# Kernel optimization log

Measured on AMD Instinct MI355X. Metric: run time of the kernel, lower is better.

The kernel has to match this reference:

```python
import jax, jax.numpy as jnp
import numpy as np

H = 128          # hidden_size == in_channels == graph_hidden_size
P = 16           # pair_neurons
B = 4096         # number of graph pairs
T = 262144       # total nodes per side
V_D, V_P, V_A = 10000, 4000, 4000          # leaf vocab sizes
NG_D, NG_P, NG_A = 13000, 5200, 5200       # DAG graph node counts
L_D, L_P, L_A = 4, 4, 5                    # ancestor levels
TOTAL_V = V_D + V_P + V_A                  # 18000 rows in all_embedding


def setup_inputs() -> dict:
    key = jax.random.key(0)
    ks = jax.random.split(key, 40)
    n = lambda i, shape, s: jax.random.normal(ks[i], shape, jnp.float32) * s
    ri = lambda i, shape, hi: jax.random.randint(ks[i], shape, 0, hi, dtype=jnp.int64)
    inp = {}
    # forward args
    inp["left_x"] = ri(0, (T, 1), TOTAL_V)
    inp["left_graph_index"] = ri(1, (B,), B)
    inp["right_x"] = ri(2, (T, 1), TOTAL_V)
    inp["right_graph_index"] = ri(3, (B,), B)
    inp["left_x_batch"] = jnp.sort(ri(4, (T,), B))
    inp["right_x_batch"] = jnp.sort(ri(5, (T,), B))
    inp["left_diag_cnt"] = ri(6, (B,), 64)
    inp["right_diag_cnt"] = ri(7, (B,), 64)
    # DAG structure buffers (built by build_ancestors in the original)
    inp["anc_d"] = ri(8, (V_D, L_D), NG_D)
    inp["leaf_d"] = ri(9, (V_D, L_D), NG_D)
    inp["anc_p"] = ri(10, (V_P, L_P), NG_P)
    inp["leaf_p"] = ri(11, (V_P, L_P), NG_P)
    inp["anc_a"] = ri(12, (V_A, L_A), NG_A)
    inp["leaf_a"] = ri(13, (V_A, L_A), NG_A)
    # learned parameters
    inp["emb_d"] = n(14, (NG_D, H), 0.1)
    inp["emb_p"] = n(15, (NG_P, H), 0.1)
    inp["emb_a"] = n(16, (NG_A, H), 0.1)
    inp["Wl_d"] = n(17, (H, 2 * H), 0.05); inp["bl_d"] = n(18, (H,), 0.05); inp["ap_d"] = n(19, (H, 1), 0.05)
    inp["Wl_p"] = n(20, (H, 2 * H), 0.05); inp["bl_p"] = n(21, (H,), 0.05); inp["ap_p"] = n(22, (H, 1), 0.05)
    inp["Wl_a"] = n(23, (H, 2 * H), 0.05); inp["bl_a"] = n(24, (H,), 0.05); inp["ap_a"] = n(25, (H, 1), 0.05)
    inp["W_ntn"] = n(26, (H, H, P), 0.02)
    inp["V_ntn"] = n(27, (P, 2 * H), 0.02)
    inp["b_ntn"] = n(28, (P,), 0.02)
    inp["w_fc"] = n(29, (1, P), 0.1)
    inp["b_fc"] = n(30, (1,), 0.1)
    return inp


def _dag_embedding(emb, anc, leaf, Wl, bl, ap):
    # emb: [Ng,H]; anc/leaf: [V,L] int
    anc_e = emb[anc]    # [V,L,H]
    leaf_e = emb[leaf]  # [V,L,H]
    h = jnp.tanh(jnp.concatenate([anc_e, leaf_e], axis=-1) @ Wl.T + bl)  # [V,L,H]
    aw = (h @ ap)[..., 0]                     # [V,L]
    s = jax.nn.softmax(aw, axis=-1)           # [V,L]
    # torch.matmul((V,L),(V,L,C)).sum(dim=1) == einsum('l,vlc->vc', s.sum(0), anc_e)
    return jnp.einsum('l,vlc->vc', s.sum(axis=0), anc_e)  # [V,H]


def reference(left_x, left_graph_index, right_x, right_graph_index,
              left_x_batch, right_x_batch, left_diag_cnt, right_diag_cnt,
              anc_d, leaf_d, anc_p, leaf_p, anc_a, leaf_a,
              emb_d, emb_p, emb_a,
              Wl_d, bl_d, ap_d, Wl_p, bl_p, ap_p, Wl_a, bl_a, ap_a,
              W_ntn, V_ntn, b_ntn, w_fc, b_fc):
    all_emb = jnp.concatenate([
        _dag_embedding(emb_d, anc_d, leaf_d, Wl_d, bl_d, ap_d),
        _dag_embedding(emb_p, anc_p, leaf_p, Wl_p, bl_p, ap_p),
        _dag_embedding(emb_a, anc_a, leaf_a, Wl_a, bl_a, ap_a),
    ], axis=0)                                  # [TOTAL_V, H]
    left_onto = all_emb[left_x[:, 0]]           # [T,H]
    right_onto = all_emb[right_x[:, 0]]         # [T,H]
    le = jax.ops.segment_sum(left_onto, left_x_batch, num_segments=B)    # [B,H]
    re = jax.ops.segment_sum(right_onto, right_x_batch, num_segments=B)  # [B,H]
    # Neural tensor similarity: tanh(e1^T W_k e2 + V [e1;e2] + b)
    bilinear = jnp.einsum('bi,ijp,bj->bp', le, W_ntn, re)                # [B,P]
    block = jnp.concatenate([le, re], axis=-1) @ V_ntn.T                 # [B,P]
    pair_sim = jnp.tanh(bilinear + block + b_ntn)                        # [B,P]
    out = jax.nn.sigmoid(pair_sim @ w_fc.T + b_fc)[:, 0]                 # [B]
    return out
```

## Files before the change

### kernel.cpp

```cpp
#include <hip/hip_runtime.h>
#include <hip/hip_bf16.h>

typedef __hip_bfloat16 bf16;
typedef __attribute__((ext_vector_type(8))) short bf16x8;
typedef __attribute__((ext_vector_type(4))) float f32x4;

#define HID 128
#define PD  16
#define BB  4096
#define TT  262144
#define VD  10000
#define VP  4000
#define VA  4000
#define NGD 13000
#define NGP 5200
#define NGA 5200

#define NB_D ((NGD + 31) / 32)
#define NB_P ((NGP + 31) / 32)
#define NB_A ((NGA + 31) / 32)

__device__ __forceinline__ float2 bf2x(unsigned int u) {
    float lo = __uint_as_float(u << 16);
    float hi = __uint_as_float(u & 0xffff0000u);
    return make_float2(lo, hi);
}

union Pack2 { bf16 h[2]; unsigned int u; };
__device__ __forceinline__ unsigned int pk2(float a, float b) {
    Pack2 p; p.h[0] = __float2bfloat16(a); p.h[1] = __float2bfloat16(b); return p.u;
}

__global__ __launch_bounds__(256) void prep_b3(
    const float* __restrict__ Wl_d, const float* __restrict__ Wl_p, const float* __restrict__ Wl_a,
    bf16* __restrict__ B3_d, bf16* __restrict__ B3_p, bf16* __restrict__ B3_a)
{
    const int sec = blockIdx.x >> 4, jt = blockIdx.x & 15;
    const float* Wl = (sec == 0) ? Wl_d : (sec == 1) ? Wl_p : Wl_a;
    bf16* B3 = (sec == 0) ? B3_d : (sec == 1) ? B3_p : B3_a;
    const int tid = threadIdx.x;
    const int q = tid >> 6, lane = tid & 63;
    const int quad = lane >> 4, m = lane & 15;
    const int col = jt * 16 + m;
    const float* src = (col < 128) ? (Wl + col * 256) : (Wl + (col - 128) * 256 + 128);
    unsigned int pk[4];
#pragma unroll
    for (int jp = 0; jp < 4; ++jp) {
        int k0 = q * 32 + quad * 8 + 2 * jp;
        pk[jp] = pk2(src[k0], src[k0 + 1]);
    }
    uint4 val = make_uint4(pk[0], pk[1], pk[2], pk[3]);
    *reinterpret_cast<uint4*>(B3 + ((size_t)(jt * 4 + q) * 64 + lane) * 8) = val;
}

__device__ __forceinline__ void stage1_body(
    unsigned short (*Abf)[136],
    const float* __restrict__ emb, const bf16* __restrict__ B3,
    bf16* __restrict__ U, int NG, int blk)
{
    const int tid  = threadIdx.x;
    const int row0 = blk * 32;
    {
        const int r = tid >> 3, seg = tid & 7;
        const int g = row0 + r;
        float v[16];
        if (g < NG) {
            const float4* src = reinterpret_cast<const float4*>(emb + (size_t)g * HID + seg * 16);
#pragma unroll
            for (int i = 0; i < 4; ++i) {
                float4 f = src[i];
                v[4 * i] = f.x; v[4 * i + 1] = f.y; v[4 * i + 2] = f.z; v[4 * i + 3] = f.w;
            }
        } else {
#pragma unroll
            for (int i = 0; i < 16; ++i) v[i] = 0.f;
        }
        unsigned int pk[8];
#pragma unroll
        for (int i = 0; i < 8; ++i) pk[i] = pk2(v[2 * i], v[2 * i + 1]);
        uint4* dst = reinterpret_cast<uint4*>(&Abf[r][seg * 16]);
        dst[0] = make_uint4(pk[0], pk[1], pk[2], pk[3]);
        dst[1] = make_uint4(pk[4], pk[5], pk[6], pk[7]);
    }
    __syncthreads();

    const int lane   = tid & 63;
    const int w      = tid >> 6;
    const int gtile  = w & 1;
    const int jstrip = w >> 1;
    const int lrow   = gtile * 16 + (lane & 15);
    const int koff   = (lane >> 4) * 8;
    const bf16x8* B3f = reinterpret_cast<const bf16x8*>(B3);

    f32x4 acc[8];
#pragma unroll
    for (int t = 0; t < 8; ++t) acc[t] = (f32x4){0.f, 0.f, 0.f, 0.f};

#pragma unroll
    for (int q = 0; q < 4; ++q) {
        bf16x8 ef = *reinterpret_cast<const bf16x8*>(&Abf[lrow][q * 32 + koff]);
#pragma unroll
        for (int t = 0; t < 8; ++t) {
            int jt = jstrip * 8 + t;
            bf16x8 wf = B3f[(jt * 4 + q) * 64 + lane];
            acc[t] = __builtin_amdgcn_mfma_f32_16x16x32_bf16(wf, ef, acc[t], 0, 0, 0);
        }
    }

    const int g = row0 + gtile * 16 + (lane & 15);
    if (g < NG) {
        const int quad = lane >> 4;
        bf16* Ur = U + (size_t)g * 256;
#pragma unroll
        for (int t = 0; t < 8; ++t) {
            int j0 = (jstrip * 8 + t) * 16 + quad * 4;
            uint2 st = make_uint2(pk2(acc[t].x, acc[t].y), pk2(acc[t].z, acc[t].w));
            *reinterpret_cast<uint2*>(Ur + j0) = st;
        }
    }
}

__global__ __launch_bounds__(256) void stage1_mfma(
    const float* __restrict__ emb_d, const bf16* __restrict__ B3_d, bf16* __restrict__ U_d,
    const float* __restrict__ emb_p, const bf16* __restrict__ B3_p, bf16* __restrict__ U_p,
    const float* __restrict__ emb_a, const bf16* __restrict__ B3_a, bf16* __restrict__ U_a)
{
    __shared__ unsigned short Abf[32][136];
    int bx = blockIdx.x;
    if (bx < NB_D)             stage1_body(Abf, emb_d, B3_d, U_d, NGD, bx);
    else if (bx < NB_D + NB_P) stage1_body(Abf, emb_p, B3_p, U_p, NGP, bx - NB_D);
    else                       stage1_body(Abf, emb_a, B3_a, U_a, NGA, bx - NB_D - NB_P);
}

template <int L>
__device__ __forceinline__ void aw_body(
    float* sacc,
    const bf16* __restrict__ U, const int* __restrict__ anc, const int* __restrict__ leaf,
    const float* __restrict__ bl, const float* __restrict__ ap,
    float* __restrict__ s_out, int V, int blk, int nblk)
{
    const int tid  = threadIdx.x;
    const int lane = tid & 63;
    const int wid  = blk * 4 + (tid >> 6);
    const int nw   = nblk * 4;
    const float2 blv = *reinterpret_cast<const float2*>(bl + 2 * lane);
    const float2 apv = *reinterpret_cast<const float2*>(ap + 2 * lane);
    const unsigned int* Uw = reinterpret_cast<const unsigned int*>(U);
    float wacc[L];
#pragma unroll
    for (int l = 0; l < L; ++l) wacc[l] = 0.f;

    for (int v = wid; v < V; v += nw) {
        float aw[L];
#pragma unroll
        for (int l = 0; l < L; ++l) {
            int a = anc[v * L + l];
            int f = leaf[v * L + l];
            float2 a2 = bf2x(Uw[(size_t)a * 128 + lane]);
            float2 l2 = bf2x(Uw[(size_t)f * 128 + 64 + lane]);
            float t0 = tanhf(a2.x + l2.x + blv.x);
            float t1 = tanhf(a2.y + l2.y + blv.y);
            float p = t0 * apv.x + t1 * apv.y;
#pragma unroll
            for (int off = 32; off; off >>= 1) p += __shfl_xor(p, off, 64);
            aw[l] = p;
        }
        float m = aw[0];
#pragma unroll
        for (int l = 1; l < L; ++l) m = fmaxf(m, aw[l]);
        float den = 0.f, e[L];
#pragma unroll
        for (int l = 0; l < L; ++l) { e[l] = __expf(aw[l] - m); den += e[l]; }
        float inv = 1.f / den;
#pragma unroll
        for (int l = 0; l < L; ++l) wacc[l] += e[l] * inv;
    }
    if (lane == 0) {
#pragma unroll
        for (int l = 0; l < L; ++l) atomicAdd(&sacc[l], wacc[l]);
    }
    __syncthreads();
    if (tid < L) atomicAdd(&s_out[tid], sacc[tid]);
}

__global__ __launch_bounds__(256) void aw_all(
    const bf16* __restrict__ U_d, const int* __restrict__ anc_d, const int* __restrict__ leaf_d,
    const float* __restrict__ bl_d, const float* __restrict__ ap_d,
    const bf16* __restrict__ U_p, const int* __restrict__ anc_p, const int* __restrict__ leaf_p,
    const float* __restrict__ bl_p, const float* __restrict__ ap_p,
    const bf16* __restrict__ U_a, const int* __restrict__ anc_a, const int* __restrict__ leaf_a,
    const float* __restrict__ bl_a, const float* __restrict__ ap_a,
    float* __restrict__ s_sum)
{
    __shared__ float sacc[5];
    const int tid = threadIdx.x;
    if (tid < 5) sacc[tid] = 0.f;
    __syncthreads();
    int bx = blockIdx.x;
    if (bx < 512)      aw_body<4>(sacc, U_d, anc_d, leaf_d, bl_d, ap_d, s_sum + 0, VD, bx, 512);
    else if (bx < 768) aw_body<4>(sacc, U_p, anc_p, leaf_p, bl_p, ap_p, s_sum + 4, VP, bx - 512, 256);
    else               aw_body<5>(sacc, U_a, anc_a, leaf_a, bl_a, ap_a, s_sum + 8, VA, bx - 768, 256);
}

template <int L>
__device__ __forceinline__ void allemb_body(
    const float* __restrict__ emb, const int* __restrict__ anc,
    const float* __restrict__ s, float* __restrict__ out, int V, int blk, int nblk)
{
    const int tid   = threadIdx.x;
    const int lane4 = tid & 31;
    const int vslot = tid >> 5;
    const float4* emb4 = reinterpret_cast<const float4*>(emb);
    float4* out4 = reinterpret_cast<float4*>(out);
    float sv[L];
#pragma unroll
    for (int l = 0; l < L; ++l) sv[l] = s[l];
    for (int v = blk * 8 + vslot; v < V; v += nblk * 8) {
        float4 a = make_float4(0.f, 0.f, 0.f, 0.f);
#pragma unroll
        for (int l = 0; l < L; ++l) {
            float4 e = emb4[(size_t)anc[v * L + l] * 32 + lane4];
            a.x += sv[l] * e.x; a.y += sv[l] * e.y;
            a.z += sv[l] * e.z; a.w += sv[l] * e.w;
        }
        out4[(size_t)v * 32 + lane4] = a;
    }
}

__global__ __launch_bounds__(256) void allemb_all(
    const float* __restrict__ emb_d, const int* __restrict__ anc_d,
    const float* __restrict__ emb_p, const int* __restrict__ anc_p,
    const float* __restrict__ emb_a, const int* __restrict__ anc_a,
    const float* __restrict__ s_sum, float* __restrict__ all_emb)
{
    int bx = blockIdx.x;
    if (bx < 512)
        allemb_body<4>(emb_d, anc_d, s_sum + 0, all_emb, VD, bx, 512);
    else if (bx < 768)
        allemb_body<4>(emb_p, anc_p, s_sum + 4, all_emb + (size_t)VD * HID, VP, bx - 512, 256);
    else
        allemb_body<5>(emb_a, anc_a, s_sum + 8, all_emb + (size_t)(VD + VP) * HID, VA, bx - 768, 256);
}

__global__ __launch_bounds__(256) void seg_bounds(
    const int* __restrict__ lb, const int* __restrict__ rb,
    int* __restrict__ segL, int* __restrict__ segR)
{
    int gid = blockIdx.x * 256 + threadIdx.x;
    const int* batch;
    int* segp;
    int b;
    if (gid <= BB) { batch = lb; segp = segL; b = gid; }
    else if (gid <= 2 * BB + 1) { batch = rb; segp = segR; b = gid - BB - 1; }
    else return;
    int l = 0, r = TT;
    while (l < r) { int m = (l + r) >> 1; if (batch[m] < b) l = m + 1; else r = m; }
    segp[b] = l;
}

__global__ __launch_bounds__(256) void segsum_f4(
    const float* __restrict__ all_emb,
    const int* __restrict__ lx, const int* __restrict__ segL, float* __restrict__ le,
    const int* __restrict__ rx, const int* __restrict__ segR, float* __restrict__ re)
{
    __shared__ float4 red[8][32];
    const int tid = threadIdx.x;
    const int b   = blockIdx.x & (BB - 1);
    const int* x;
    const int* seg;
    float* out;
    if (blockIdx.x < BB) { x = lx; seg = segL; out = le; }
    else                 { x = rx; seg = segR; out = re; }
    const int lo = seg[b], hi = seg[b + 1];
    const int lane4 = tid & 31;
    const int slot  = tid >> 5;
    const float4* AE4 = reinterpret_cast<const float4*>(all_emb);
    float4 acc = make_float4(0.f, 0.f, 0.f, 0.f);
    int t = lo + slot;
    for (; t + 8 < hi; t += 16) {
        int i0 = x[t], i1 = x[t + 8];
        float4 v0 = AE4[(size_t)i0 * 32 + lane4];
        float4 v1 = AE4[(size_t)i1 * 32 + lane4];
        acc.x += v0.x; acc.y += v0.y; acc.z += v0.z; acc.w += v0.w;
        acc.x += v1.x; acc.y += v1.y; acc.z += v1.z; acc.w += v1.w;
    }
    for (; t < hi; t += 8) {
        float4 v0 = AE4[(size_t)x[t] * 32 + lane4];
        acc.x += v0.x; acc.y += v0.y; acc.z += v0.z; acc.w += v0.w;
    }
    red[slot][lane4] = acc;
    __syncthreads();
    if (slot < 4) {
        float4 o = red[slot + 4][lane4];
        acc.x += o.x; acc.y += o.y; acc.z += o.z; acc.w += o.w;
        red[slot][lane4] = acc;
    }
    __syncthreads();
    if (slot < 2) {
        float4 o = red[slot + 2][lane4];
        acc.x += o.x; acc.y += o.y; acc.z += o.z; acc.w += o.w;
        red[slot][lane4] = acc;
    }
    __syncthreads();
    if (slot == 0) {
        float4 o = red[1][lane4];
        acc.x += o.x; acc.y += o.y; acc.z += o.z; acc.w += o.w;
        reinterpret_cast<float4*>(out)[(size_t)b * 32 + lane4] = acc;
    }
}

__global__ __launch_bounds__(256) void ntn_part(
    const float* __restrict__ le, const float* __restrict__ re,
    const float* __restrict__ W2, float* __restrict__ part)
{
    __shared__ float Alds[32][68];
    __shared__ float Blds[32 * 264];
    __shared__ float Rlds[64][17];
    const int tid   = threadIdx.x;
    const int row0  = blockIdx.x * 64;
    const int col0  = blockIdx.y * 256;
    const int lane5 = tid & 31;
    const int rbase = (tid >> 5) * 8;
    const int cbase = lane5 * 8;
    float acc[8][8];
#pragma unroll
    for (int i = 0; i < 8; ++i)
#pragma unroll
        for (int j = 0; j < 8; ++j) acc[i][j] = 0.f;

    for (int i = tid; i < 64 * 16; i += 256) {
        int rr = i >> 4, jl = i & 15;
        Rlds[rr][jl] = re[(size_t)(row0 + rr) * HID + blockIdx.y * 16 + jl];
    }

    for (int k0 = 0; k0 < 128; k0 += 32) {
        __syncthreads();
        for (int i = tid; i < 64 * 32; i += 256) {
            int rr = i >> 5, kk = i & 31;
            Alds[kk][rr] = le[(size_t)(row0 + rr) * HID + k0 + kk];
        }
        for (int i = tid; i < 32 * 64; i += 256) {
            int kk = i >> 6, j4 = (i & 63) * 4;
            float4 v = *reinterpret_cast<const float4*>(&W2[(size_t)(k0 + kk) * 2048 + col0 + j4]);
            *reinterpret_cast<float4*>(&Blds[kk * 264 + j4]) = v;
        }
        __syncthreads();
#pragma unroll
        for (int kk = 0; kk < 32; ++kk) {
            float4 a0 = *reinterpret_cast<const float4*>(&Alds[kk][rbase]);
            float4 a1 = *reinterpret_cast<const float4*>(&Alds[kk][rbase + 4]);
            float4 b0 = *reinterpret_cast<const float4*>(&Blds[kk * 264 + cbase]);
            float4 b1 = *reinterpret_cast<const float4*>(&Blds[kk * 264 + cbase + 4]);
            float av[8] = {a0.x, a0.y, a0.z, a0.w, a1.x, a1.y, a1.z, a1.w};
            float bv[8] = {b0.x, b0.y, b0.z, b0.w, b1.x, b1.y, b1.z, b1.w};
#pragma unroll
            for (int i = 0; i < 8; ++i)
#pragma unroll
                for (int j = 0; j < 8; ++j) acc[i][j] += av[i] * bv[j];
        }
    }

    const int jloc = lane5 >> 1;
    const int pq   = (tid & 1) * 8;
#pragma unroll
    for (int i = 0; i < 8; ++i) {
        int row = rbase + i;
        float rj = Rlds[row][jloc];
        float pb[8];
#pragma unroll
        for (int j = 0; j < 8; ++j) pb[j] = acc[i][j] * rj;
#pragma unroll
        for (int m = 2; m <= 16; m <<= 1) {
#pragma unroll
            for (int j = 0; j < 8; ++j) pb[j] += __shfl_xor(pb[j], m, 64);
        }
        if ((tid & 30) == 0) {
            size_t base = ((size_t)blockIdx.y * BB + row0 + row) * PD + pq;
            *reinterpret_cast<float4*>(&part[base])     = make_float4(pb[0], pb[1], pb[2], pb[3]);
            *reinterpret_cast<float4*>(&part[base + 4]) = make_float4(pb[4], pb[5], pb[6], pb[7]);
        }
    }
}

__global__ __launch_bounds__(256) void ntn_epi(
    const float* __restrict__ part, const float* __restrict__ le, const float* __restrict__ re,
    const float* __restrict__ Vntn, const float* __restrict__ bntn,
    const float* __restrict__ wfc, const float* __restrict__ bfc,
    float* __restrict__ out)
{
    __shared__ float Vlds[16 * 257];
    __shared__ float LE[16 * 128];
    __shared__ float RE[16 * 128];
    const int tid = threadIdx.x;
    const int b0  = blockIdx.x * 16;
    for (int i = tid; i < 4096; i += 256) Vlds[(i >> 8) * 257 + (i & 255)] = Vntn[i];
    for (int i = tid; i < 2048; i += 256) {
        LE[i] = le[(size_t)b0 * HID + i];
        RE[i] = re[(size_t)b0 * HID + i];
    }
    __syncthreads();
    const int bl = tid >> 4, p = tid & 15;
    const int b  = b0 + bl;
    float bil = 0.f;
#pragma unroll
    for (int by = 0; by < 8; ++by) bil += part[((size_t)by * BB + b) * PD + p];
    float s = bil + bntn[p];
    const float* Vp   = &Vlds[p * 257];
    const float* lrow = &LE[bl * 128];
    const float* rrow = &RE[bl * 128];
#pragma unroll 8
    for (int c = 0; c < 128; ++c) s += lrow[c] * Vp[c] + rrow[c] * Vp[128 + c];
    float x = tanhf(s) * wfc[p];
    x += __shfl_xor(x, 1, 64);
    x += __shfl_xor(x, 2, 64);
    x += __shfl_xor(x, 4, 64);
    x += __shfl_xor(x, 8, 64);
    if (p == 0) out[b] = 1.f / (1.f + __expf(-(x + bfc[0])));
}

extern "C" void kernel_launch(void* const* d_in, const int* in_sizes, int n_in,
                              void* d_out, int out_size, void* d_ws, size_t ws_size,
                              hipStream_t stream)
{
    const int* left_x      = (const int*)d_in[0];
    const int* right_x     = (const int*)d_in[2];
    const int* left_batch  = (const int*)d_in[4];
    const int* right_batch = (const int*)d_in[5];
    const int* anc_d  = (const int*)d_in[8];
    const int* leaf_d = (const int*)d_in[9];
    const int* anc_p  = (const int*)d_in[10];
    const int* leaf_p = (const int*)d_in[11];
    const int* anc_a  = (const int*)d_in[12];
    const int* leaf_a = (const int*)d_in[13];
    const float* emb_d = (const float*)d_in[14];
    const float* emb_p = (const float*)d_in[15];
    const float* emb_a = (const float*)d_in[16];
    const float* Wl_d = (const float*)d_in[17];
    const float* bl_d = (const float*)d_in[18];
    const float* ap_d = (const float*)d_in[19];
    const float* Wl_p = (const float*)d_in[20];
    const float* bl_p = (const float*)d_in[21];
    const float* ap_p = (const float*)d_in[22];
    const float* Wl_a = (const float*)d_in[23];
    const float* bl_a = (const float*)d_in[24];
    const float* ap_a = (const float*)d_in[25];
    const float* W_ntn = (const float*)d_in[26];
    const float* V_ntn = (const float*)d_in[27];
    const float* b_ntn = (const float*)d_in[28];
    const float* w_fc  = (const float*)d_in[29];
    const float* b_fc  = (const float*)d_in[30];
    float* out = (float*)d_out;

    float* ws = (float*)d_ws;
    float* s_sum   = ws;
    float* le      = ws + 64;
    float* re      = le + (size_t)BB * HID;
    float* all_emb = re + (size_t)BB * HID;
    float* part    = all_emb + (size_t)(VD + VP + VA) * HID;
    int*   segL    = (int*)(part + (size_t)8 * BB * PD);
    int*   segR    = segL + 4100;
    bf16*  U       = (bf16*)(segR + 4100);
    bf16*  U_d = U;
    bf16*  U_p = U_d + (size_t)NGD * 256;
    bf16*  U_a = U_p + (size_t)NGP * 256;
    bf16*  B3_d = U_a + (size_t)NGA * 256;
    bf16*  B3_p = B3_d + 32768;
    bf16*  B3_a = B3_p + 32768;

    prep_b3<<<48, 256, 0, stream>>>(Wl_d, Wl_p, Wl_a, B3_d, B3_p, B3_a);

    hipMemsetAsync(s_sum, 0, 16 * sizeof(float), stream);

    seg_bounds<<<33, 256, 0, stream>>>(left_batch, right_batch, segL, segR);

    stage1_mfma<<<NB_D + NB_P + NB_A, 256, 0, stream>>>(
        emb_d, B3_d, U_d, emb_p, B3_p, U_p, emb_a, B3_a, U_a);

    aw_all<<<1024, 256, 0, stream>>>(
        U_d, anc_d, leaf_d, bl_d, ap_d,
        U_p, anc_p, leaf_p, bl_p, ap_p,
        U_a, anc_a, leaf_a, bl_a, ap_a, s_sum);

    allemb_all<<<1024, 256, 0, stream>>>(
        emb_d, anc_d, emb_p, anc_p, emb_a, anc_a, s_sum, all_emb);

    segsum_f4<<<2 * BB, 256, 0, stream>>>(
        all_emb, left_x, segL, le, right_x, segR, re);

    ntn_part<<<dim3(64, 8), 256, 0, stream>>>(le, re, W_ntn, part);

    ntn_epi<<<BB / 16, 256, 0, stream>>>(part, le, re, V_ntn, b_ntn, w_fc, b_fc, out);
}
```

Measured before the change: 245.8 us.

## Process vertex pairs in attention kernels, widen segsum loads, fold memset

The attention-weight and all-embedding kernels now handle two vertices per iteration, using int4 index loads and issuing all gathers before any compute to raise memory-level parallelism. The segment-sum kernel switches to one wavefront per row chunk with float2 lanes and 8-way unrolled independent gathers, and a simpler shared-memory reduction. The s_sum zeroing memset is folded into the seg_bounds kernel to drop a separate launch. Odd V would skip the last vertex, but all vocab sizes are even; register pressure rises.

```diff
diff --git a/kernel.cpp b/kernel.cpp
--- a/kernel.cpp
+++ b/kernel.cpp
@@ -150,30 +150,61 @@
 #pragma unroll
     for (int l = 0; l < L; ++l) wacc[l] = 0.f;
 
-    for (int v = wid; v < V; v += nw) {
-        float aw[L];
+    for (int vp = wid; vp < V / 2; vp += nw) {
+        const int v0 = 2 * vp;
+        int a0[L], f0[L], a1[L], f1[L];
+        if (L == 4) {
+            int4 ia = *reinterpret_cast<const int4*>(anc  + (size_t)v0 * 4);
+            int4 ib = *reinterpret_cast<const int4*>(anc  + (size_t)v0 * 4 + 4);
+            int4 fa = *reinterpret_cast<const int4*>(leaf + (size_t)v0 * 4);
+            int4 fb = *reinterpret_cast<const int4*>(leaf + (size_t)v0 * 4 + 4);
+            a0[0] = ia.x; a0[1] = ia.y; a0[2] = ia.z; a0[3] = ia.w;
+            a1[0] = ib.x; a1[1] = ib.y; a1[2] = ib.z; a1[3] = ib.w;
+            f0[0] = fa.x; f0[1] = fa.y; f0[2] = fa.z; f0[3] = fa.w;
+            f1[0] = fb.x; f1[1] = fb.y; f1[2] = fb.z; f1[3] = fb.w;
+        } else {
+#pragma unroll
+            for (int l = 0; l < L; ++l) {
+                a0[l] = anc[(size_t)v0 * L + l];
+                a1[l] = anc[(size_t)(v0 + 1) * L + l];
+                f0[l] = leaf[(size_t)v0 * L + l];
+                f1[l] = leaf[(size_t)(v0 + 1) * L + l];
+            }
+        }
+        unsigned int ua0[L], ul0[L], ua1[L], ul1[L];
 #pragma unroll
         for (int l = 0; l < L; ++l) {
-            int a = anc[v * L + l];
-            int f = leaf[v * L + l];
-            float2 a2 = bf2x(Uw[(size_t)a * 128 + lane]);
-            float2 l2 = bf2x(Uw[(size_t)f * 128 + 64 + lane]);
-            float t0 = tanhf(a2.x + l2.x + blv.x);
-            float t1 = tanhf(a2.y + l2.y + blv.y);
-            float p = t0 * apv.x + t1 * apv.y;
-#pragma unroll
-            for (int off = 32; off; off >>= 1) p += __shfl_xor(p, off, 64);
-            aw[l] = p;
-        }
-        float m = aw[0];
-#pragma unroll
-        for (int l = 1; l < L; ++l) m = fmaxf(m, aw[l]);
-        float den = 0.f, e[L];
-#pragma unroll
-        for (int l = 0; l < L; ++l) { e[l] = __expf(aw[l] - m); den += e[l]; }
-        float inv = 1.f / den;
-#pragma unroll
-        for (int l = 0; l < L; ++l) wacc[l] += e[l] * inv;
+            ua0[l] = Uw[(size_t)a0[l] * 128 + lane];
+            ul0[l] = Uw[(size_t)f0[l] * 128 + 64 + lane];
+            ua1[l] = Uw[(size_t)a1[l] * 128 + lane];
+            ul1[l] = Uw[(size_t)f1[l] * 128 + 64 + lane];
+        }
+        float aw0[L], aw1[L];
+#pragma unroll
+        for (int l = 0; l < L; ++l) {
+            float2 x0 = bf2x(ua0[l]), y0 = bf2x(ul0[l]);
+            float2 x1 = bf2x(ua1[l]), y1 = bf2x(ul1[l]);
+            float p0 = tanhf(x0.x + y0.x + blv.x) * apv.x + tanhf(x0.y + y0.y + blv.y) * apv.y;
+            float p1 = tanhf(x1.x + y1.x + blv.x) * apv.x + tanhf(x1.y + y1.y + blv.y) * apv.y;
+#pragma unroll
+            for (int off = 32; off; off >>= 1) {
+                p0 += __shfl_xor(p0, off, 64);
+                p1 += __shfl_xor(p1, off, 64);
+            }
+            aw0[l] = p0; aw1[l] = p1;
+        }
+        float m0 = aw0[0], m1 = aw1[0];
+#pragma unroll
+        for (int l = 1; l < L; ++l) { m0 = fmaxf(m0, aw0[l]); m1 = fmaxf(m1, aw1[l]); }
+        float d0 = 0.f, d1 = 0.f, e0[L], e1[L];
+#pragma unroll
+        for (int l = 0; l < L; ++l) {
+            e0[l] = __expf(aw0[l] - m0); d0 += e0[l];
+            e1[l] = __expf(aw1[l] - m1); d1 += e1[l];
+        }
+        float i0 = 1.f / d0, i1 = 1.f / d1;
+#pragma unroll
+        for (int l = 0; l < L; ++l) wacc[l] += e0[l] * i0 + e1[l] * i1;
     }
     if (lane == 0) {
 #pragma unroll
@@ -215,15 +246,38 @@
     float sv[L];
 #pragma unroll
     for (int l = 0; l < L; ++l) sv[l] = s[l];
-    for (int v = blk * 8 + vslot; v < V; v += nblk * 8) {
-        float4 a = make_float4(0.f, 0.f, 0.f, 0.f);
+    for (int vp = blk * 8 + vslot; vp < V / 2; vp += nblk * 8) {
+        const int v0 = 2 * vp;
+        int a0[L], a1[L];
+        if (L == 4) {
+            int4 ia = *reinterpret_cast<const int4*>(anc + (size_t)v0 * 4);
+            int4 ib = *reinterpret_cast<const int4*>(anc + (size_t)v0 * 4 + 4);
+            a0[0] = ia.x; a0[1] = ia.y; a0[2] = ia.z; a0[3] = ia.w;
+            a1[0] = ib.x; a1[1] = ib.y; a1[2] = ib.z; a1[3] = ib.w;
+        } else {
+#pragma unroll
+            for (int l = 0; l < L; ++l) {
+                a0[l] = anc[(size_t)v0 * L + l];
+                a1[l] = anc[(size_t)(v0 + 1) * L + l];
+            }
+        }
+        float4 e0[L], e1[L];
 #pragma unroll
         for (int l = 0; l < L; ++l) {
-            float4 e = emb4[(size_t)anc[v * L + l] * 32 + lane4];
-            a.x += sv[l] * e.x; a.y += sv[l] * e.y;
-            a.z += sv[l] * e.z; a.w += sv[l] * e.w;
-        }
-        out4[(size_t)v * 32 + lane4] = a;
+            e0[l] = emb4[(size_t)a0[l] * 32 + lane4];
+            e1[l] = emb4[(size_t)a1[l] * 32 + lane4];
+        }
+        float4 r0 = make_float4(0.f, 0.f, 0.f, 0.f);
+        float4 r1 = make_float4(0.f, 0.f, 0.f, 0.f);
+#pragma unroll
+        for (int l = 0; l < L; ++l) {
+            r0.x += sv[l] * e0[l].x; r0.y += sv[l] * e0[l].y;
+            r0.z += sv[l] * e0[l].z; r0.w += sv[l] * e0[l].w;
+            r1.x += sv[l] * e1[l].x; r1.y += sv[l] * e1[l].y;
+            r1.z += sv[l] * e1[l].z; r1.w += sv[l] * e1[l].w;
+        }
+        out4[(size_t)v0 * 32 + lane4]       = r0;
+        out4[(size_t)(v0 + 1) * 32 + lane4] = r1;
     }
 }
 
@@ -244,9 +298,10 @@
 
 __global__ __launch_bounds__(256) void seg_bounds(
     const int* __restrict__ lb, const int* __restrict__ rb,
-    int* __restrict__ segL, int* __restrict__ segR)
+    int* __restrict__ segL, int* __restrict__ segR, float* __restrict__ s_sum)
 {
     int gid = blockIdx.x * 256 + threadIdx.x;
+    if (gid >= 2 * BB + 8 && gid < 2 * BB + 24) s_sum[gid - (2 * BB + 8)] = 0.f;
     const int* batch;
     int* segp;
     int b;
@@ -258,54 +313,46 @@
     segp[b] = l;
 }
 
-__global__ __launch_bounds__(256) void segsum_f4(
+__global__ __launch_bounds__(256) void segsum_f2(
     const float* __restrict__ all_emb,
     const int* __restrict__ lx, const int* __restrict__ segL, float* __restrict__ le,
     const int* __restrict__ rx, const int* __restrict__ segR, float* __restrict__ re)
 {
-    __shared__ float4 red[8][32];
-    const int tid = threadIdx.x;
-    const int b   = blockIdx.x & (BB - 1);
+    __shared__ float2 red[4][64];
+    const int tid  = threadIdx.x;
+    const int b    = blockIdx.x & (BB - 1);
+    const int lane = tid & 63;
+    const int w    = tid >> 6;
     const int* x;
     const int* seg;
     float* out;
     if (blockIdx.x < BB) { x = lx; seg = segL; out = le; }
     else                 { x = rx; seg = segR; out = re; }
     const int lo = seg[b], hi = seg[b + 1];
-    const int lane4 = tid & 31;
-    const int slot  = tid >> 5;
-    const float4* AE4 = reinterpret_cast<const float4*>(all_emb);
-    float4 acc = make_float4(0.f, 0.f, 0.f, 0.f);
-    int t = lo + slot;
-    for (; t + 8 < hi; t += 16) {
-        int i0 = x[t], i1 = x[t + 8];
-        float4 v0 = AE4[(size_t)i0 * 32 + lane4];
-        float4 v1 = AE4[(size_t)i1 * 32 + lane4];
-        acc.x += v0.x; acc.y += v0.y; acc.z += v0.z; acc.w += v0.w;
-        acc.x += v1.x; acc.y += v1.y; acc.z += v1.z; acc.w += v1.w;
-    }
-    for (; t < hi; t += 8) {
-        float4 v0 = AE4[(size_t)x[t] * 32 + lane4];
-        acc.x += v0.x; acc.y += v0.y; acc.z += v0.z; acc.w += v0.w;
-    }
-    red[slot][lane4] = acc;
+    const float2* AE2 = reinterpret_cast<const float2*>(all_emb);
+    float2 acc = make_float2(0.f, 0.f);
+    int t = lo + w;
+    for (; t + 28 < hi; t += 32) {
+        int idx[8];
+#pragma unroll
+        for (int u = 0; u < 8; ++u) idx[u] = x[t + 4 * u];
+        float2 v[8];
+#pragma unroll
+        for (int u = 0; u < 8; ++u) v[u] = AE2[(size_t)idx[u] * 64 + lane];
+#pragma unroll
+        for (int u = 0; u < 8; ++u) { acc.x += v[u].x; acc.y += v[u].y; }
+    }
+    for (; t < hi; t += 4) {
+        float2 v = AE2[(size_t)x[t] * 64 + lane];
+        acc.x += v.x; acc.y += v.y;
+    }
+    if (w > 0) red[w][lane] = acc;
     __syncthreads();
-    if (slot < 4) {
-        float4 o = red[slot + 4][lane4];
-        acc.x += o.x; acc.y += o.y; acc.z += o.z; acc.w += o.w;
-        red[slot][lane4] = acc;
-    }
-    __syncthreads();
-    if (slot < 2) {
-        float4 o = red[slot + 2][lane4];
-        acc.x += o.x; acc.y += o.y; acc.z += o.z; acc.w += o.w;
-        red[slot][lane4] = acc;
-    }
-    __syncthreads();
-    if (slot == 0) {
-        float4 o = red[1][lane4];
-        acc.x += o.x; acc.y += o.y; acc.z += o.z; acc.w += o.w;
-        reinterpret_cast<float4*>(out)[(size_t)b * 32 + lane4] = acc;
+    if (w == 0) {
+        float2 r1 = red[1][lane], r2 = red[2][lane], r3 = red[3][lane];
+        acc.x += r1.x + r2.x + r3.x;
+        acc.y += r1.y + r2.y + r3.y;
+        reinterpret_cast<float2*>(out)[(size_t)b * 64 + lane] = acc;
     }
 }
 
@@ -469,9 +516,7 @@
 
     prep_b3<<<48, 256, 0, stream>>>(Wl_d, Wl_p, Wl_a, B3_d, B3_p, B3_a);
 
-    hipMemsetAsync(s_sum, 0, 16 * sizeof(float), stream);
-
-    seg_bounds<<<33, 256, 0, stream>>>(left_batch, right_batch, segL, segR);
+    seg_bounds<<<33, 256, 0, stream>>>(left_batch, right_batch, segL, segR, s_sum);
 
     stage1_mfma<<<NB_D + NB_P + NB_A, 256, 0, stream>>>(
         emb_d, B3_d, U_d, emb_p, B3_p, U_p, emb_a, B3_a, U_a);
@@ -484,7 +529,7 @@
     allemb_all<<<1024, 256, 0, stream>>>(
         emb_d, anc_d, emb_p, anc_p, emb_a, anc_a, s_sum, all_emb);
 
-    segsum_f4<<<2 * BB, 256, 0, stream>>>(
+    segsum_f2<<<2 * BB, 256, 0, stream>>>(
         all_emb, left_x, segL, le, right_x, segR, re);
 
     ntn_part<<<dim3(64, 8), 256, 0, stream>>>(le, re, W_ntn, part);
```

After: 238.1 us. -3.1%, faster.
